# Performance work log

Measured on AMD Instinct MI355X. Metric: run time of the kernel, lower is better.

The kernel has to match this reference:

```python
import jax, jax.numpy as jnp
import numpy as np

B, S, D, H = 4, 2048, 1024, 16
HD = D // H
DFF = 4 * D
EPS = 1e-5


def setup_inputs() -> dict:
    key = jax.random.key(0)
    ks = jax.random.split(key, 8)
    s = 0.02
    return {
        "x": jax.random.normal(ks[0], (B, S, D), dtype=jnp.float32),
        "ln1_g": jnp.ones((D,), jnp.float32),
        "ln1_b": jnp.zeros((D,), jnp.float32),
        "Wq": jax.random.normal(ks[1], (D, D), jnp.float32) * s,
        "Wk": jax.random.normal(ks[2], (D, D), jnp.float32) * s,
        "Wv": jax.random.normal(ks[3], (D, D), jnp.float32) * s,
        "Wo": jax.random.normal(ks[4], (D, D), jnp.float32) * s,
        "ln2_g": jnp.ones((D,), jnp.float32),
        "ln2_b": jnp.zeros((D,), jnp.float32),
        "W1": jax.random.normal(ks[5], (D, DFF), jnp.float32) * s,
        "b1": jnp.zeros((DFF,), jnp.float32),
        "W2": jax.random.normal(ks[6], (DFF, D), jnp.float32) * s,
        "b2": jnp.zeros((D,), jnp.float32),
    }


def _layernorm(x, g, b):
    mu = jnp.mean(x, axis=-1, keepdims=True)
    var = jnp.var(x, axis=-1, keepdims=True)
    return (x - mu) * jax.lax.rsqrt(var + EPS) * g + b


def _block(x, ln1_g, ln1_b, Wq, Wk, Wv, Wo, ln2_g, ln2_b, W1, b1, W2, b2):
    # --- attention sub-block (pre-norm) ---
    h = _layernorm(x, ln1_g, ln1_b)
    q = (h @ Wq).reshape(B, S, H, HD)
    k = (h @ Wk).reshape(B, S, H, HD)
    v = (h @ Wv).reshape(B, S, H, HD)
    scores = jnp.einsum("bqhd,bkhd->bhqk", q, k) / np.sqrt(HD).astype(np.float32)
    causal = jnp.tril(jnp.ones((S, S), dtype=bool))
    scores = jnp.where(causal, scores, -jnp.inf)
    attn = jax.nn.softmax(scores, axis=-1)  # dropout p=0 (eval)
    ctx = jnp.einsum("bhqk,bkhd->bqhd", attn, v).reshape(B, S, D)
    x = x + ctx @ Wo
    # --- FFN sub-block (pre-norm) ---
    h = _layernorm(x, ln2_g, ln2_b)
    h = jax.nn.gelu(h @ W1 + b1, approximate=False)  # torch nn.GELU() = exact erf
    return x + (h @ W2 + b2)


def reference(x, ln1_g, ln1_b, Wq, Wk, Wv, Wo, ln2_g, ln2_b, W1, b1, W2, b2):
    return _block(x, ln1_g, ln1_b, Wq, Wk, Wv, Wo, ln2_g, ln2_b, W1, b1, W2, b2)
```

## Files before the change

kernel.cpp:

```cpp
#include <hip/hip_runtime.h>
#include <hip/hip_bf16.h>
#include <math.h>

#define NB 4
#define NS 2048
#define ND 1024
#define NH 16
#define NHD 64
#define NDFF 4096
#define QKS 3072

typedef __attribute__((ext_vector_type(8))) short bf16x8;
typedef __attribute__((ext_vector_type(4))) float f32x4;
typedef __attribute__((ext_vector_type(16))) float f32x16;
typedef __attribute__((ext_vector_type(4))) short short4v;
typedef __attribute__((ext_vector_type(4))) int i32x4;

static __device__ __forceinline__ short f2b(float f) {
  union { __hip_bfloat16 b; short s; } u;
  u.b = __float2bfloat16(f);
  return u.s;
}

static __device__ __forceinline__ int cvtpk(float lo, float hi_) {
  int r;
  asm("v_cvt_pk_bf16_f32 %0, %1, %2" : "=v"(r) : "v"(lo), "v"(hi_));
  return r;
}

static __device__ __forceinline__ float pairmax(float x) {
  auto r = __builtin_amdgcn_permlane32_swap(__float_as_uint(x), __float_as_uint(x), false, false);
  return fmaxf(__uint_as_float(r[0]), __uint_as_float(r[1]));
}
static __device__ __forceinline__ float pairsum(float x) {
  auto r = __builtin_amdgcn_permlane32_swap(__float_as_uint(x), __float_as_uint(x), false, false);
  return __uint_as_float(r[0]) + __uint_as_float(r[1]);
}

__global__ __launch_bounds__(256) void ln_kernel(
    const float* __restrict__ x, const float* __restrict__ g,
    const float* __restrict__ b, short* __restrict__ out) {
  __shared__ float red[8];
  const int row = blockIdx.x;
  const int t = threadIdx.x;
  const float* xr = x + (size_t)row * ND;
  const float4 xv = *(const float4*)(xr + t * 4);
  float s = xv.x + xv.y + xv.z + xv.w;
  float ss = xv.x * xv.x + xv.y * xv.y + xv.z * xv.z + xv.w * xv.w;
#pragma unroll
  for (int m = 32; m >= 1; m >>= 1) {
    s += __shfl_xor(s, m);
    ss += __shfl_xor(ss, m);
  }
  if ((t & 63) == 0) { red[(t >> 6) * 2] = s; red[(t >> 6) * 2 + 1] = ss; }
  __syncthreads();
  s = red[0] + red[2] + red[4] + red[6];
  ss = red[1] + red[3] + red[5] + red[7];
  const float mu = s * (1.0f / ND);
  const float var = ss * (1.0f / ND) - mu * mu;
  const float rs = rsqrtf(var + 1e-5f);
  const float4 gv = *(const float4*)(g + t * 4);
  const float4 bv = *(const float4*)(b + t * 4);
  short o[4];
  o[0] = f2b((xv.x - mu) * rs * gv.x + bv.x);
  o[1] = f2b((xv.y - mu) * rs * gv.y + bv.y);
  o[2] = f2b((xv.z - mu) * rs * gv.z + bv.z);
  o[3] = f2b((xv.w - mu) * rs * gv.w + bv.w);
  *(short4v*)(out + (size_t)row * ND + t * 4) = *(short4v*)o;
}

__global__ __launch_bounds__(256) void tcast_kernel(
    const float* __restrict__ in, short* __restrict__ out, int K, int N) {
  __shared__ float tile[32][33];
  const int n0 = blockIdx.x * 32, k0 = blockIdx.y * 32;
  const int tx = threadIdx.x & 31, ty = threadIdx.x >> 5;
#pragma unroll
  for (int i = 0; i < 32; i += 8)
    tile[ty + i][tx] = in[(size_t)(k0 + ty + i) * N + n0 + tx];
  __syncthreads();
#pragma unroll
  for (int i = 0; i < 32; i += 8)
    out[(size_t)(n0 + ty + i) * K + k0 + tx] = f2b(tile[tx][ty + i]);
}

__global__ __launch_bounds__(256) void vtrans_kernel(
    const short* __restrict__ in, short* __restrict__ out) {
  __shared__ short tile[64][72];
  const int s0 = blockIdx.x * 64, bh = blockIdx.y;
  const int bb = bh >> 4, hh = bh & 15;
  const int rr = threadIdx.x >> 3, cc = (threadIdx.x & 7) * 8;
#pragma unroll
  for (int it = 0; it < 2; ++it) {
    const int r = rr + it * 32;
    *(bf16x8*)&tile[r][cc] =
        *(const bf16x8*)&in[((size_t)(bb * NS + s0 + r)) * QKS + 2048 + hh * NHD + cc];
  }
  __syncthreads();
  const size_t ob = (size_t)bh * NHD * NS;
#pragma unroll
  for (int it = 0; it < 2; ++it) {
    const int d = rr + it * 32;
    short o[8];
#pragma unroll
    for (int j = 0; j < 8; ++j) o[j] = tile[cc + j][d];
    *(bf16x8*)&out[ob + (size_t)d * NS + s0 + cc] = *(bf16x8*)o;
  }
}

__device__ __forceinline__ void gload16(const void* g, void* l) {
  __builtin_amdgcn_global_load_lds(
      (const __attribute__((address_space(1))) unsigned int*)g,
      (__attribute__((address_space(3))) unsigned int*)l, 16, 0, 0);
}

template <int BN, int EPI>
__global__ __launch_bounds__(512, 2) void gemmr_kernel(
    const short* __restrict__ A, const short* __restrict__ Bt,
    float* __restrict__ Cf, short* __restrict__ Cb,
    const float* __restrict__ bias, const float* __restrict__ res,
    int M, int N, int K) {
  constexpr int MI = (BN == 256) ? 8 : 4;
  constexpr int NWN = (BN == 256) ? 4 : 2;
  constexpr int ABUF = 8192;
  constexpr int TS = ABUF + BN * 32;
  __shared__ short lds[4][TS];

  const int tid = threadIdx.x, l = tid & 63, w = tid >> 6;
  const int wm = w / NWN, wn = w % NWN;
  const int nbm = M >> 8, nbn = N / BN, nwg = nbm * nbn;
  int wg = blockIdx.x;
  wg = (wg & 7) * (nwg >> 3) + (wg >> 3);
  const int bm = wg / nbn, bn = wg % nbn;

  const int lrow = tid >> 2;
  const int sslot = (l & 3) ^ ((lrow >> 1) & 3);
  const short* Asrc = A + (size_t)(bm * 256 + lrow) * K + sslot * 8;
  const short* Bsrc = Bt + (size_t)(bn * BN + lrow) * K + sslot * 8;
  const int ldst = w * 512;

  const int fr = l & 15, fg4 = l >> 4;
  int aoff[MI], boff[4];
#pragma unroll
  for (int mi = 0; mi < MI; ++mi) {
    const int r = wm * (MI * 16) + mi * 16 + fr;
    aoff[mi] = r * 32 + ((fg4 ^ ((r >> 1) & 3)) << 3);
  }
#pragma unroll
  for (int nj = 0; nj < 4; ++nj) {
    const int r = wn * 64 + nj * 16 + fr;
    boff[nj] = ABUF + r * 32 + ((fg4 ^ ((r >> 1) & 3)) << 3);
  }

  auto stageAB = [&](int t, short* buf) {
    const short* sa = Asrc + t * 32;
    gload16(sa, buf + ldst);
    gload16(sa + (size_t)128 * K, buf + 4096 + ldst);
    const short* sb = Bsrc + t * 32;
    gload16(sb, buf + ABUF + ldst);
    if constexpr (BN == 256) gload16(sb + (size_t)128 * K, buf + ABUF + 4096 + ldst);
  };

  f32x4 acc[MI][4] = {};
  const int NT = K >> 5;

  stageAB(0, lds[0]);
  stageAB(1, lds[1]);
  stageAB(2, lds[2]);
  if constexpr (BN == 256)
    asm volatile("s_waitcnt vmcnt(8)\n\ts_barrier" ::: "memory");
  else
    asm volatile("s_waitcnt vmcnt(6)\n\ts_barrier" ::: "memory");

  for (int t = 0; t < NT; ++t) {
    const short* cur = &lds[t & 3][0];
    short* pbuf = &lds[(t + 3) & 3][0];
    const bool st = (t + 3 < NT);
    bf16x8 bfr[4], af[4];
#pragma unroll
    for (int nj = 0; nj < 4; ++nj) bfr[nj] = *(const bf16x8*)(cur + boff[nj]);
#pragma unroll
    for (int mi = 0; mi < 4; ++mi) af[mi] = *(const bf16x8*)(cur + aoff[mi]);
    if (st) stageAB(t + 3, pbuf);
    asm volatile("s_barrier" ::: "memory");
    __builtin_amdgcn_s_setprio(1);
#pragma unroll
    for (int mi = 0; mi < 4; ++mi)
#pragma unroll
      for (int nj = 0; nj < 4; ++nj)
        acc[mi][nj] = __builtin_amdgcn_mfma_f32_16x16x32_bf16(af[mi], bfr[nj], acc[mi][nj], 0, 0, 0);
    __builtin_amdgcn_s_setprio(0);
    if constexpr (BN == 256) {
      asm volatile("s_barrier" ::: "memory");
#pragma unroll
      for (int mi = 0; mi < 4; ++mi) af[mi] = *(const bf16x8*)(cur + aoff[4 + mi]);
      asm volatile("s_barrier" ::: "memory");
      __builtin_amdgcn_s_setprio(1);
#pragma unroll
      for (int mi = 0; mi < 4; ++mi)
#pragma unroll
        for (int nj = 0; nj < 4; ++nj)
          acc[4 + mi][nj] =
              __builtin_amdgcn_mfma_f32_16x16x32_bf16(af[mi], bfr[nj], acc[4 + mi][nj], 0, 0, 0);
      __builtin_amdgcn_s_setprio(0);
    }
    if (t + 3 < NT) {
      if constexpr (BN == 256)
        asm volatile("s_waitcnt vmcnt(8)\n\ts_barrier" ::: "memory");
      else
        asm volatile("s_waitcnt vmcnt(6)\n\ts_barrier" ::: "memory");
    } else if (t + 2 < NT) {
      if constexpr (BN == 256)
        asm volatile("s_waitcnt vmcnt(4)\n\ts_barrier" ::: "memory");
      else
        asm volatile("s_waitcnt vmcnt(3)\n\ts_barrier" ::: "memory");
    } else if (t + 1 < NT) {
      asm volatile("s_waitcnt vmcnt(0)\n\ts_barrier" ::: "memory");
    }
  }

  const int fq = (l >> 4) * 4;
  const int wrb = bm * 256 + wm * (MI * 16);
  const int wcb = bn * BN + wn * 64;
#pragma unroll
  for (int mi = 0; mi < MI; ++mi) {
#pragma unroll
    for (int ni = 0; ni < 4; ++ni) {
#pragma unroll
      for (int rr = 0; rr < 4; ++rr) {
        const int row = wrb + mi * 16 + fq + rr;
        const int col = wcb + ni * 16 + fr;
        float v = acc[mi][ni][rr];
        if (EPI == 0) {
          Cb[(size_t)row * N + col] = f2b(v);
        } else if (EPI == 1) {
          Cf[(size_t)row * N + col] = v + res[(size_t)row * N + col];
        } else if (EPI == 2) {
          v += bias[col];
          v = 0.5f * v * (1.0f + erff(v * 0.70710678118f));
          Cb[(size_t)row * N + col] = f2b(v);
        } else {
          Cf[(size_t)row * N + col] = v + bias[col] + res[(size_t)row * N + col];
        }
      }
    }
  }
}

__global__ __launch_bounds__(256, 2) void attn_kernel(
    const short* __restrict__ qkv, const short* __restrict__ vt, short* __restrict__ ctx) {
  __shared__ short Kls[2][64 * 64];
  __shared__ short Vls[2][64 * 64];

  const int bid = blockIdx.x;
  const int bh = (bid & 7) * 8 + ((bid >> 3) & 7);
  const int cp = bid >> 6;
  const int bb = bh >> 4, hh = bh & 15;
  const int lane = threadIdx.x & 63, wave = threadIdx.x >> 6;
  const int ql = lane & 31, hi = lane >> 5;
  const int qbA = cp * 128 + wave * 32;
  const int qbB = (15 - cp) * 128 + wave * 32;

  bf16x8 qf[2][4];
#pragma unroll
  for (int hf = 0; hf < 2; ++hf) {
    const int qb0 = hf ? qbB : qbA;
    const size_t qrow = ((size_t)bb * NS + qb0 + ql) * QKS + hh * NHD;
#pragma unroll
    for (int st = 0; st < 4; ++st)
      qf[hf][st] = *(const bf16x8*)&qkv[qrow + st * 16 + hi * 8];
  }

  f32x16 acc[2][2] = {};
  float m_run[2] = {-1e37f, -1e37f};
  float l_run[2] = {0.f, 0.f};

  const int srow = lane >> 3;
  const int sslot = (lane & 7) ^ srow;
  const short* kbasep = qkv + (size_t)bb * NS * QKS + 1024 + hh * NHD + sslot * 8;
  const short* vbasep = vt + (size_t)bh * NHD * NS + sslot * 8;

  const int nkt = (16 - cp) * 2;
#pragma unroll
  for (int r = 0; r < 2; ++r) {
    const int row = r * 32 + wave * 8 + srow;
    gload16(kbasep + (size_t)row * QKS, &Kls[0][(r * 32 + wave * 8) * 64]);
    gload16(vbasep + (size_t)row * NS, &Vls[0][(r * 32 + wave * 8) * 64]);
  }

  int buf = 0;
  for (int jt = 0; jt < nkt; ++jt) {
    asm volatile("s_waitcnt vmcnt(0)\n\ts_barrier" ::: "memory");
    if (jt + 1 < nkt) {
      const int k0n = (jt + 1) * 64;
#pragma unroll
      for (int r = 0; r < 2; ++r) {
        const int row = r * 32 + wave * 8 + srow;
        gload16(kbasep + (size_t)(k0n + row) * QKS, &Kls[buf ^ 1][(r * 32 + wave * 8) * 64]);
        gload16(vbasep + (size_t)row * NS + k0n, &Vls[buf ^ 1][(r * 32 + wave * 8) * 64]);
      }
    }
    const int k0 = jt * 64;
    const short* Kb = &Kls[buf][0];
    const short* Vb = &Vls[buf][0];
#pragma unroll
    for (int ks = 0; ks < 2; ++ks) {
      const int kbase = k0 + ks * 32;
      if (kbase > qbB) continue;
      bf16x8 kf[4], vf[2][2];
      const int krow = ks * 32 + ql;
#pragma unroll
      for (int st = 0; st < 4; ++st)
        kf[st] = *(const bf16x8*)&Kb[krow * 64 + ((st * 2 + hi) ^ (krow & 7)) * 8];
#pragma unroll
      for (int db = 0; db < 2; ++db) {
        const int vrow = db * 32 + ql;
#pragma unroll
        for (int su = 0; su < 2; ++su)
          vf[db][su] =
              *(const bf16x8*)&Vb[vrow * 64 + ((ks * 4 + su * 2 + hi) ^ (vrow & 7)) * 8];
      }
#pragma unroll
      for (int hf = 0; hf < 2; ++hf) {
        const int qb0 = hf ? qbB : qbA;
        if (kbase > qb0) continue;
        const int qg = qb0 + ql;
        f32x16 s = {};
        __builtin_amdgcn_s_setprio(1);
#pragma unroll
        for (int st = 0; st < 4; ++st)
          s = __builtin_amdgcn_mfma_f32_32x32x16_bf16(kf[st], qf[hf][st], s, 0, 0, 0);
        __builtin_amdgcn_s_setprio(0);
        const bool masked = (kbase + 31 > qb0);
        float pv[16];
        float mt = -INFINITY;
#pragma unroll
        for (int r = 0; r < 16; ++r) {
          float v = s[r] * 0.125f;
          if (masked) {
            const int key = kbase + 4 * hi + (r & 3) + 8 * (r >> 2);
            v = (key > qg) ? -INFINITY : v;
          }
          pv[r] = v;
          mt = fmaxf(mt, v);
        }
        mt = pairmax(mt);
        if (!__all(mt - m_run[hf] <= 8.0f)) {
          const float mn = fmaxf(m_run[hf], mt);
          const float sc = __expf(m_run[hf] - mn);
          m_run[hf] = mn;
          l_run[hf] *= sc;
          acc[hf][0] *= sc;
          acc[hf][1] *= sc;
        }
        float pe[16];
        float lt = 0.f;
#pragma unroll
        for (int r = 0; r < 16; ++r) {
          pe[r] = __expf(fminf(pv[r] - m_run[hf], 80.0f));
          lt += pe[r];
        }
        l_run[hf] += pairsum(lt);
        bf16x8 pf[2];
#pragma unroll
        for (int su = 0; su < 2; ++su) {
          const int a0 = cvtpk(pe[su * 8 + 0], pe[su * 8 + 1]);
          const int a1 = cvtpk(pe[su * 8 + 2], pe[su * 8 + 3]);
          const int b0 = cvtpk(pe[su * 8 + 4], pe[su * 8 + 5]);
          const int b1 = cvtpk(pe[su * 8 + 6], pe[su * 8 + 7]);
          auto r0 = __builtin_amdgcn_permlane32_swap((unsigned)a0, (unsigned)b0, false, false);
          auto r1 = __builtin_amdgcn_permlane32_swap((unsigned)a1, (unsigned)b1, false, false);
          union { i32x4 w; bf16x8 v; } u;
          u.w[0] = r0[0]; u.w[1] = r1[0]; u.w[2] = r0[1]; u.w[3] = r1[1];
          pf[su] = u.v;
        }
        __builtin_amdgcn_s_setprio(1);
#pragma unroll
        for (int su = 0; su < 2; ++su) {
          acc[hf][0] = __builtin_amdgcn_mfma_f32_32x32x16_bf16(vf[0][su], pf[su], acc[hf][0], 0, 0, 0);
          acc[hf][1] = __builtin_amdgcn_mfma_f32_32x32x16_bf16(vf[1][su], pf[su], acc[hf][1], 0, 0, 0);
        }
        __builtin_amdgcn_s_setprio(0);
      }
    }
    asm volatile("s_waitcnt lgkmcnt(0)\n\ts_barrier" ::: "memory");
    buf ^= 1;
  }

#pragma unroll
  for (int hf = 0; hf < 2; ++hf) {
    const int qb0 = hf ? qbB : qbA;
    const float inv = 1.0f / l_run[hf];
    const size_t ob = ((size_t)bb * NS + qb0 + ql) * ND + hh * NHD + hi * 8;
#pragma unroll
    for (int db = 0; db < 2; ++db) {
#pragma unroll
      for (int J = 0; J < 2; ++J) {
        const int a0 = cvtpk(acc[hf][db][J * 8 + 0] * inv, acc[hf][db][J * 8 + 1] * inv);
        const int a1 = cvtpk(acc[hf][db][J * 8 + 2] * inv, acc[hf][db][J * 8 + 3] * inv);
        const int b0 = cvtpk(acc[hf][db][J * 8 + 4] * inv, acc[hf][db][J * 8 + 5] * inv);
        const int b1 = cvtpk(acc[hf][db][J * 8 + 6] * inv, acc[hf][db][J * 8 + 7] * inv);
        auto r0 = __builtin_amdgcn_permlane32_swap((unsigned)a0, (unsigned)b0, false, false);
        auto r1 = __builtin_amdgcn_permlane32_swap((unsigned)a1, (unsigned)b1, false, false);
        union { i32x4 w; bf16x8 v; } u;
        u.w[0] = r0[0]; u.w[1] = r1[0]; u.w[2] = r0[1]; u.w[3] = r1[1];
        *(bf16x8*)&ctx[ob + db * 32 + J * 16] = u.v;
      }
    }
  }
}

extern "C" void kernel_launch(void* const* d_in, const int* in_sizes, int n_in,
                              void* d_out, int out_size, void* d_ws, size_t ws_size,
                              hipStream_t stream) {
  (void)in_sizes; (void)n_in; (void)out_size; (void)ws_size;
  const float* x     = (const float*)d_in[0];
  const float* ln1_g = (const float*)d_in[1];
  const float* ln1_b = (const float*)d_in[2];
  const float* Wq    = (const float*)d_in[3];
  const float* Wk    = (const float*)d_in[4];
  const float* Wv    = (const float*)d_in[5];
  const float* Wo    = (const float*)d_in[6];
  const float* ln2_g = (const float*)d_in[7];
  const float* ln2_b = (const float*)d_in[8];
  const float* W1    = (const float*)d_in[9];
  const float* b1    = (const float*)d_in[10];
  const float* W2    = (const float*)d_in[11];
  const float* b2    = (const float*)d_in[12];
  float* out = (float*)d_out;

  char* ws = (char*)d_ws;
  const size_t MiB = 1024 * 1024;
  short* wqkvT = (short*)(ws + 0 * MiB);
  short* woT   = (short*)(ws + 6 * MiB);
  short* w1T   = (short*)(ws + 8 * MiB);
  short* w2T   = (short*)(ws + 16 * MiB);
  short* h     = (short*)(ws + 24 * MiB);
  short* ctx   = (short*)(ws + 24 * MiB);
  short* qkv   = (short*)(ws + 40 * MiB);
  short* vt    = (short*)(ws + 88 * MiB);
  short* hff   = (short*)(ws + 40 * MiB);
  float* x1    = (float*)(ws + 104 * MiB);

  tcast_kernel<<<dim3(32, 32), 256, 0, stream>>>(Wq, wqkvT, 1024, 1024);
  tcast_kernel<<<dim3(32, 32), 256, 0, stream>>>(Wk, wqkvT + 1024 * 1024, 1024, 1024);
  tcast_kernel<<<dim3(32, 32), 256, 0, stream>>>(Wv, wqkvT + 2048 * 1024, 1024, 1024);
  tcast_kernel<<<dim3(32, 32), 256, 0, stream>>>(Wo, woT, 1024, 1024);
  tcast_kernel<<<dim3(128, 32), 256, 0, stream>>>(W1, w1T, 1024, 4096);
  tcast_kernel<<<dim3(32, 128), 256, 0, stream>>>(W2, w2T, 4096, 1024);

  ln_kernel<<<8192, 256, 0, stream>>>(x, ln1_g, ln1_b, h);

  gemmr_kernel<128, 0><<<768, 512, 0, stream>>>(h, wqkvT, nullptr, qkv, nullptr, nullptr,
                                                8192, 3072, 1024);
  vtrans_kernel<<<dim3(32, 64), 256, 0, stream>>>(qkv, vt);

  attn_kernel<<<512, 256, 0, stream>>>(qkv, vt, ctx);

  gemmr_kernel<128, 1><<<256, 512, 0, stream>>>(ctx, woT, x1, nullptr, nullptr, x,
                                                8192, 1024, 1024);

  ln_kernel<<<8192, 256, 0, stream>>>(x1, ln2_g, ln2_b, h);

  gemmr_kernel<256, 2><<<512, 512, 0, stream>>>(h, w1T, nullptr, hff, b1, nullptr,
                                                8192, 4096, 1024);
  gemmr_kernel<128, 3><<<256, 512, 0, stream>>>(hff, w2T, out, nullptr, b2, x1,
                                                8192, 1024, 4096);
}
```

Measured before the change: 387.9 us.

## Restructure GEMM into double-buffered BK=64 ping-pong with split A/B staging

Replaces the 4-stage BK=32 LDS pipeline with a 2-buffer BK=64 scheme in which each K-step is split into four phases. Each phase loads A or B fragments, issues a partial prefetch of the next tile, and runs half the MFMAs, so loads interleave with compute at finer grain. The warp layout is generalized (NWN=BN/64), so the BN=256 variant now uses 8 MI rows per wave without a second A reload. The QKV projection switches from BN=128 to BN=256 with half the workgroups. This adds more barriers per iteration and changes LDS footprint and occupancy.

```diff
diff --git a/kernel.cpp b/kernel.cpp
--- a/kernel.cpp
+++ b/kernel.cpp
@@ -15,6 +15,11 @@
 typedef __attribute__((ext_vector_type(16))) float f32x16;
 typedef __attribute__((ext_vector_type(4))) short short4v;
 typedef __attribute__((ext_vector_type(4))) int i32x4;
+
+#define BAR() asm volatile("s_barrier" ::: "memory")
+#define VMBAR4() asm volatile("s_waitcnt vmcnt(4)\n\ts_barrier" ::: "memory")
+#define VMBAR3() asm volatile("s_waitcnt vmcnt(3)\n\ts_barrier" ::: "memory")
+#define VMBAR0() asm volatile("s_waitcnt vmcnt(0)\n\ts_barrier" ::: "memory")
 
 static __device__ __forceinline__ short f2b(float f) {
   union { __hip_bfloat16 b; short s; } u;
@@ -114,16 +119,18 @@
 }
 
 template <int BN, int EPI>
-__global__ __launch_bounds__(512, 2) void gemmr_kernel(
+__global__ __launch_bounds__(512, 2) void gemm8p_kernel(
     const short* __restrict__ A, const short* __restrict__ Bt,
     float* __restrict__ Cf, short* __restrict__ Cb,
     const float* __restrict__ bias, const float* __restrict__ res,
     int M, int N, int K) {
-  constexpr int MI = (BN == 256) ? 8 : 4;
-  constexpr int NWN = (BN == 256) ? 4 : 2;
-  constexpr int ABUF = 8192;
-  constexpr int TS = ABUF + BN * 32;
-  __shared__ short lds[4][TS];
+  constexpr int NWN = BN / 64;
+  constexpr int NWM = 8 / NWN;
+  constexpr int MI = 256 / (NWM * 16);
+  constexpr int AU = 256 * 32;
+  constexpr int BU = BN * 32;
+  constexpr int TS = 2 * (AU + BU);
+  __shared__ short lds[2][TS];
 
   const int tid = threadIdx.x, l = tid & 63, w = tid >> 6;
   const int wm = w / NWN, wn = w % NWN;
@@ -132,11 +139,24 @@
   wg = (wg & 7) * (nwg >> 3) + (wg >> 3);
   const int bm = wg / nbn, bn = wg % nbn;
 
-  const int lrow = tid >> 2;
-  const int sslot = (l & 3) ^ ((lrow >> 1) & 3);
-  const short* Asrc = A + (size_t)(bm * 256 + lrow) * K + sslot * 8;
-  const short* Bsrc = Bt + (size_t)(bn * BN + lrow) * K + sslot * 8;
-  const int ldst = w * 512;
+  const int arow = tid >> 2;
+  const int aslot = (l & 3) ^ ((arow >> 1) & 3);
+  const short* Asrc = A + (size_t)(bm * 256 + arow) * K + aslot * 8;
+  const short* Bsrc = Bt + (size_t)(bn * BN + arow) * K + aslot * 8;
+  const int wdst = w * 512;
+
+  auto stA = [&](int t, int kh, short* buf) {
+    const short* s = Asrc + (size_t)t * 64 + kh * 32;
+    short* d = buf + kh * AU + wdst;
+    gload16(s, d);
+    gload16(s + (size_t)128 * K, d + 4096);
+  };
+  auto stB = [&](int t, int kh, short* buf) {
+    const short* s = Bsrc + (size_t)t * 64 + kh * 32;
+    short* d = buf + 2 * AU + kh * BU + wdst;
+    gload16(s, d);
+    if constexpr (BN == 256) gload16(s + (size_t)128 * K, d + 4096);
+  };
 
   const int fr = l & 15, fg4 = l >> 4;
   int aoff[MI], boff[4];
@@ -148,74 +168,80 @@
 #pragma unroll
   for (int nj = 0; nj < 4; ++nj) {
     const int r = wn * 64 + nj * 16 + fr;
-    boff[nj] = ABUF + r * 32 + ((fg4 ^ ((r >> 1) & 3)) << 3);
-  }
-
-  auto stageAB = [&](int t, short* buf) {
-    const short* sa = Asrc + t * 32;
-    gload16(sa, buf + ldst);
-    gload16(sa + (size_t)128 * K, buf + 4096 + ldst);
-    const short* sb = Bsrc + t * 32;
-    gload16(sb, buf + ABUF + ldst);
-    if constexpr (BN == 256) gload16(sb + (size_t)128 * K, buf + ABUF + 4096 + ldst);
-  };
+    boff[nj] = 2 * AU + r * 32 + ((fg4 ^ ((r >> 1) & 3)) << 3);
+  }
 
   f32x4 acc[MI][4] = {};
-  const int NT = K >> 5;
-
-  stageAB(0, lds[0]);
-  stageAB(1, lds[1]);
-  stageAB(2, lds[2]);
-  if constexpr (BN == 256)
-    asm volatile("s_waitcnt vmcnt(8)\n\ts_barrier" ::: "memory");
-  else
-    asm volatile("s_waitcnt vmcnt(6)\n\ts_barrier" ::: "memory");
+  const int NT = K >> 6;
+
+  {
+    short* b0 = (short*)&lds[0][0];
+    stA(0, 0, b0); stB(0, 0, b0); stA(0, 1, b0); stB(0, 1, b0);
+  }
+  if constexpr (BN == 256) VMBAR4(); else VMBAR3();
 
   for (int t = 0; t < NT; ++t) {
-    const short* cur = &lds[t & 3][0];
-    short* pbuf = &lds[(t + 3) & 3][0];
-    const bool st = (t + 3 < NT);
-    bf16x8 bfr[4], af[4];
-#pragma unroll
-    for (int nj = 0; nj < 4; ++nj) bfr[nj] = *(const bf16x8*)(cur + boff[nj]);
-#pragma unroll
-    for (int mi = 0; mi < 4; ++mi) af[mi] = *(const bf16x8*)(cur + aoff[mi]);
-    if (st) stageAB(t + 3, pbuf);
-    asm volatile("s_barrier" ::: "memory");
+    const short* cur = &lds[t & 1][0];
+    short* nxt = (short*)&lds[(t + 1) & 1][0];
+    const bool pf = (t + 1 < NT);
+    bf16x8 af[MI], q0, q1;
+
+#pragma unroll
+    for (int mi = 0; mi < MI; ++mi) af[mi] = *(const bf16x8*)(cur + aoff[mi]);
+    q0 = *(const bf16x8*)(cur + boff[0]);
+    q1 = *(const bf16x8*)(cur + boff[1]);
+    if (pf) stA(t + 1, 0, nxt);
+    BAR();
     __builtin_amdgcn_s_setprio(1);
 #pragma unroll
-    for (int mi = 0; mi < 4; ++mi)
-#pragma unroll
-      for (int nj = 0; nj < 4; ++nj)
-        acc[mi][nj] = __builtin_amdgcn_mfma_f32_16x16x32_bf16(af[mi], bfr[nj], acc[mi][nj], 0, 0, 0);
+    for (int mi = 0; mi < MI; ++mi) {
+      acc[mi][0] = __builtin_amdgcn_mfma_f32_16x16x32_bf16(af[mi], q0, acc[mi][0], 0, 0, 0);
+      acc[mi][1] = __builtin_amdgcn_mfma_f32_16x16x32_bf16(af[mi], q1, acc[mi][1], 0, 0, 0);
+    }
     __builtin_amdgcn_s_setprio(0);
-    if constexpr (BN == 256) {
-      asm volatile("s_barrier" ::: "memory");
-#pragma unroll
-      for (int mi = 0; mi < 4; ++mi) af[mi] = *(const bf16x8*)(cur + aoff[4 + mi]);
-      asm volatile("s_barrier" ::: "memory");
-      __builtin_amdgcn_s_setprio(1);
-#pragma unroll
-      for (int mi = 0; mi < 4; ++mi)
-#pragma unroll
-        for (int nj = 0; nj < 4; ++nj)
-          acc[4 + mi][nj] =
-              __builtin_amdgcn_mfma_f32_16x16x32_bf16(af[mi], bfr[nj], acc[4 + mi][nj], 0, 0, 0);
-      __builtin_amdgcn_s_setprio(0);
-    }
-    if (t + 3 < NT) {
-      if constexpr (BN == 256)
-        asm volatile("s_waitcnt vmcnt(8)\n\ts_barrier" ::: "memory");
-      else
-        asm volatile("s_waitcnt vmcnt(6)\n\ts_barrier" ::: "memory");
-    } else if (t + 2 < NT) {
-      if constexpr (BN == 256)
-        asm volatile("s_waitcnt vmcnt(4)\n\ts_barrier" ::: "memory");
-      else
-        asm volatile("s_waitcnt vmcnt(3)\n\ts_barrier" ::: "memory");
-    } else if (t + 1 < NT) {
-      asm volatile("s_waitcnt vmcnt(0)\n\ts_barrier" ::: "memory");
-    }
+    BAR();
+
+    q0 = *(const bf16x8*)(cur + boff[2]);
+    q1 = *(const bf16x8*)(cur + boff[3]);
+    if (pf) stB(t + 1, 0, nxt);
+    BAR();
+    __builtin_amdgcn_s_setprio(1);
+#pragma unroll
+    for (int mi = 0; mi < MI; ++mi) {
+      acc[mi][2] = __builtin_amdgcn_mfma_f32_16x16x32_bf16(af[mi], q0, acc[mi][2], 0, 0, 0);
+      acc[mi][3] = __builtin_amdgcn_mfma_f32_16x16x32_bf16(af[mi], q1, acc[mi][3], 0, 0, 0);
+    }
+    __builtin_amdgcn_s_setprio(0);
+    if (pf) { if constexpr (BN == 256) VMBAR4(); else VMBAR3(); }
+    else VMBAR0();
+
+#pragma unroll
+    for (int mi = 0; mi < MI; ++mi) af[mi] = *(const bf16x8*)(cur + AU + aoff[mi]);
+    q0 = *(const bf16x8*)(cur + BU + boff[0]);
+    q1 = *(const bf16x8*)(cur + BU + boff[1]);
+    if (pf) stA(t + 1, 1, nxt);
+    BAR();
+    __builtin_amdgcn_s_setprio(1);
+#pragma unroll
+    for (int mi = 0; mi < MI; ++mi) {
+      acc[mi][0] = __builtin_amdgcn_mfma_f32_16x16x32_bf16(af[mi], q0, acc[mi][0], 0, 0, 0);
+      acc[mi][1] = __builtin_amdgcn_mfma_f32_16x16x32_bf16(af[mi], q1, acc[mi][1], 0, 0, 0);
+    }
+    __builtin_amdgcn_s_setprio(0);
+    BAR();
+
+    q0 = *(const bf16x8*)(cur + BU + boff[2]);
+    q1 = *(const bf16x8*)(cur + BU + boff[3]);
+    if (pf) stB(t + 1, 1, nxt);
+    BAR();
+    __builtin_amdgcn_s_setprio(1);
+#pragma unroll
+    for (int mi = 0; mi < MI; ++mi) {
+      acc[mi][2] = __builtin_amdgcn_mfma_f32_16x16x32_bf16(af[mi], q0, acc[mi][2], 0, 0, 0);
+      acc[mi][3] = __builtin_amdgcn_mfma_f32_16x16x32_bf16(af[mi], q1, acc[mi][3], 0, 0, 0);
+    }
+    __builtin_amdgcn_s_setprio(0);
+    if constexpr (BN == 256) VMBAR4(); else VMBAR3();
   }
 
   const int fq = (l >> 4) * 4;
@@ -289,7 +315,7 @@
 
   int buf = 0;
   for (int jt = 0; jt < nkt; ++jt) {
-    asm volatile("s_waitcnt vmcnt(0)\n\ts_barrier" ::: "memory");
+    VMBAR0();
     if (jt + 1 < nkt) {
       const int k0n = (jt + 1) * 64;
 #pragma unroll
@@ -450,19 +476,19 @@
 
   ln_kernel<<<8192, 256, 0, stream>>>(x, ln1_g, ln1_b, h);
 
-  gemmr_kernel<128, 0><<<768, 512, 0, stream>>>(h, wqkvT, nullptr, qkv, nullptr, nullptr,
-                                                8192, 3072, 1024);
+  gemm8p_kernel<256, 0><<<384, 512, 0, stream>>>(h, wqkvT, nullptr, qkv, nullptr, nullptr,
+                                                 8192, 3072, 1024);
   vtrans_kernel<<<dim3(32, 64), 256, 0, stream>>>(qkv, vt);
 
   attn_kernel<<<512, 256, 0, stream>>>(qkv, vt, ctx);
 
-  gemmr_kernel<128, 1><<<256, 512, 0, stream>>>(ctx, woT, x1, nullptr, nullptr, x,
-                                                8192, 1024, 1024);
+  gemm8p_kernel<128, 1><<<256, 512, 0, stream>>>(ctx, woT, x1, nullptr, nullptr, x,
+                                                 8192, 1024, 1024);
 
   ln_kernel<<<8192, 256, 0, stream>>>(x1, ln2_g, ln2_b, h);
 
-  gemmr_kernel<256, 2><<<512, 512, 0, stream>>>(h, w1T, nullptr, hff, b1, nullptr,
-                                                8192, 4096, 1024);
-  gemmr_kernel<128, 3><<<256, 512, 0, stream>>>(hff, w2T, out, nullptr, b2, x1,
-                                                8192, 1024, 4096);
-}
+  gemm8p_kernel<256, 2><<<512, 512, 0, stream>>>(h, w1T, nullptr, hff, b1, nullptr,
+                                                 8192, 4096, 1024);
+  gemm8p_kernel<128, 3><<<256, 512, 0, stream>>>(hff, w2T, out, nullptr, b2, x1,
+                                                 8192, 1024, 4096);
+}
```

Measured after the change: 393.3 us. Within noise of the previous version (+1.4%).
